# Performance work log

Measured on AMD Instinct MI355X. Metric: run time of the kernel, lower is better.

## Reference

```python
import jax, jax.numpy as jnp
import numpy as np


def setup_inputs() -> dict:
    key = jax.random.key(0)
    k1, k2 = jax.random.split(key)
    x = jax.random.normal(k1, (4, 11, 64, 96, 96), dtype=jnp.float32)
    gamma = jax.random.normal(k2, (1,), dtype=jnp.float32) * 0.1
    return {"x": x, "gamma": gamma}


def reference(x, gamma):
    # x: (B, N, C, H, W)
    B, N, C, H, W = x.shape
    q = x.reshape(B, N, C * H * W)  # (B, N, D)

    # Gram matrix: energy2[b,i,j] = <q_i, q_j>
    energy2 = jnp.einsum('bnd,bmd->bnm', q, q)  # (B, N, N)

    # Pairwise L1 distance energy1[b,i,j] = sum_d |q_i - q_j|.
    # Loop over small fixed N=11 rows to avoid a (B,N,N,D) intermediate.
    rows = [jnp.sum(jnp.abs(q - q[:, i:i + 1, :]), axis=-1) for i in range(N)]
    energy1 = jnp.stack(rows, axis=1)  # (B, N, N)
    # Original torch writes into energy1.data -> no gradient flows through it.
    energy1 = jax.lax.stop_gradient(energy1)

    energy = energy1 * energy2
    energy_new = jnp.max(energy, axis=-1, keepdims=True) - energy
    attention = jax.nn.softmax(energy_new, axis=-1)  # (B, N, N)

    out = jnp.einsum('bnm,bmd->bnd', attention, q)  # (B, N, D)
    out = out.reshape(B, N, C, H, W)
    out = gamma * out + x
    return out.reshape(B, N * C, H, W)
```

## Files before the change

### kernel.cpp

```cpp
#include <hip/hip_runtime.h>

#define B_    4
#define N_    11
#define D_    589824L
#define NPAIR 66
#define TPB   256
#define ITER  8

__global__ __launch_bounds__(TPB) void reduce_kernel(const float* __restrict__ x,
                                                     double* __restrict__ e2ws,
                                                     double* __restrict__ e1ws) {
    const int b = blockIdx.y;
    const int t = threadIdx.x;
    const long base = (long)blockIdx.x * (TPB * 4 * ITER) + (long)t * 4;
    const float* xb = x + (long)b * N_ * D_;

    float acc2[NPAIR];
    float acc1[NPAIR];
#pragma unroll
    for (int p = 0; p < NPAIR; ++p) { acc2[p] = 0.f; acc1[p] = 0.f; }

#pragma unroll 1
    for (int k = 0; k < ITER; ++k) {
        const long d = base + (long)k * (TPB * 4);
        float4 v[N_];
#pragma unroll
        for (int m = 0; m < N_; ++m)
            v[m] = *reinterpret_cast<const float4*>(xb + (long)m * D_ + d);

        int p = 0;
#pragma unroll
        for (int i = 0; i < N_; ++i) {
#pragma unroll
            for (int j = i; j < N_; ++j) {
                acc2[p] += v[i].x * v[j].x + v[i].y * v[j].y +
                           v[i].z * v[j].z + v[i].w * v[j].w;
                if (i != j) {
                    acc1[p] += fabsf(v[i].x - v[j].x) + fabsf(v[i].y - v[j].y) +
                               fabsf(v[i].z - v[j].z) + fabsf(v[i].w - v[j].w);
                }
                ++p;
            }
        }
    }

    __shared__ float red2[TPB / 64][NPAIR];
    __shared__ float red1[TPB / 64][NPAIR];
    const int wave = t >> 6, lane = t & 63;
#pragma unroll
    for (int p = 0; p < NPAIR; ++p) {
        float s2 = acc2[p], s1 = acc1[p];
#pragma unroll
        for (int off = 32; off > 0; off >>= 1) {
            s2 += __shfl_down(s2, off, 64);
            s1 += __shfl_down(s1, off, 64);
        }
        if (lane == 0) { red2[wave][p] = s2; red1[wave][p] = s1; }
    }
    __syncthreads();
    if (t < NPAIR) {
        float s2 = 0.f, s1 = 0.f;
#pragma unroll
        for (int w = 0; w < TPB / 64; ++w) { s2 += red2[w][t]; s1 += red1[w][t]; }
        atomicAdd(&e2ws[b * NPAIR + t], (double)s2);
        atomicAdd(&e1ws[b * NPAIR + t], (double)s1);
    }
}

__global__ __launch_bounds__(128) void attn_kernel(const double* __restrict__ e2ws,
                                                   const double* __restrict__ e1ws,
                                                   const float* __restrict__ gamma,
                                                   float* __restrict__ Mws) {
    const int b = blockIdx.x;
    const int t = threadIdx.x;
    __shared__ double E[N_][N_];
    if (t < NPAIR) {
        int rem = t, i = 0, cnt = N_;
        while (rem >= cnt) { rem -= cnt; --cnt; ++i; }
        const int j = i + rem;
        const double e = e1ws[b * NPAIR + t] * e2ws[b * NPAIR + t];
        E[i][j] = e;
        E[j][i] = e;
    }
    __syncthreads();
    if (t < N_) {
        const int i = t;
        double mn = E[i][0];
#pragma unroll
        for (int j = 1; j < N_; ++j) mn = fmin(mn, E[i][j]);
        double ex[N_], s = 0.0;
#pragma unroll
        for (int j = 0; j < N_; ++j) { ex[j] = exp(mn - E[i][j]); s += ex[j]; }
        const float g = gamma[0];
        const double inv = 1.0 / s;
#pragma unroll
        for (int j = 0; j < N_; ++j) {
            float m = (float)(ex[j] * inv) * g + (i == j ? 1.0f : 0.0f);
            Mws[(b * N_ + i) * N_ + j] = m;
        }
    }
}

__global__ __launch_bounds__(TPB) void apply_kernel(const float* __restrict__ x,
                                                    const float* __restrict__ Mws,
                                                    float* __restrict__ out) {
    const int b = blockIdx.y;
    const int t = threadIdx.x;
    __shared__ float M[N_ * N_];
    if (t < N_ * N_) M[t] = Mws[b * N_ * N_ + t];
    __syncthreads();

    const long d = (long)blockIdx.x * (TPB * 4) + (long)t * 4;
    const float* xb = x + (long)b * N_ * D_;
    float* ob = out + (long)b * N_ * D_;

    float4 v[N_];
#pragma unroll
    for (int m = 0; m < N_; ++m)
        v[m] = *reinterpret_cast<const float4*>(xb + (long)m * D_ + d);

#pragma unroll
    for (int n = 0; n < N_; ++n) {
        float4 o = make_float4(0.f, 0.f, 0.f, 0.f);
#pragma unroll
        for (int m = 0; m < N_; ++m) {
            const float w = M[n * N_ + m];
            o.x += w * v[m].x;
            o.y += w * v[m].y;
            o.z += w * v[m].z;
            o.w += w * v[m].w;
        }
        *reinterpret_cast<float4*>(ob + (long)n * D_ + d) = o;
    }
}

extern "C" void kernel_launch(void* const* d_in, const int* in_sizes, int n_in,
                              void* d_out, int out_size, void* d_ws, size_t ws_size,
                              hipStream_t stream) {
    const float* x     = (const float*)d_in[0];
    const float* gamma = (const float*)d_in[1];
    float* out         = (float*)d_out;

    double* e2ws = (double*)d_ws;
    double* e1ws = e2ws + B_ * NPAIR;
    float*  Mws  = (float*)(e1ws + B_ * NPAIR);

    hipMemsetAsync(d_ws, 0, (size_t)(2 * B_ * NPAIR) * sizeof(double), stream);

    dim3 gridA(D_ / (TPB * 4 * ITER), B_);
    reduce_kernel<<<gridA, TPB, 0, stream>>>(x, e2ws, e1ws);

    attn_kernel<<<B_, 128, 0, stream>>>(e2ws, e1ws, gamma, Mws);

    dim3 gridC(D_ / (TPB * 4), B_);
    apply_kernel<<<gridC, TPB, 0, stream>>>(x, Mws, out);
}
```

Measured before the change: 266.7 us.

## Trim L1 accumulators, use DPP wave reductions, raise occupancy, nontemporal output stores

The reduce kernel drops the 11 always-zero diagonal L1 accumulators, which cuts register pressure, and requests 3 waves per SIMD via launch bounds. ITER falls from 8 to 3, so more blocks are launched. The shuffle-based wave reductions become DPP row and broadcast operations, and the two LDS staging arrays merge into one. The apply kernel writes its output with nontemporal stores to reduce cache pollution. In exchange, the smaller ITER increases the number of global double atomics, and the attn kernel has to remap indices between the two accumulator layouts.

```diff
diff --git a/kernel.cpp b/kernel.cpp
--- a/kernel.cpp
+++ b/kernel.cpp
@@ -3,22 +3,37 @@
 #define B_    4
 #define N_    11
 #define D_    589824L
-#define NPAIR 66
+#define NP2   66
+#define NP1   55
+#define NRED  121
 #define TPB   256
-#define ITER  8
+#define ITER  3
 
-__global__ __launch_bounds__(TPB) void reduce_kernel(const float* __restrict__ x,
-                                                     double* __restrict__ e2ws,
-                                                     double* __restrict__ e1ws) {
+__device__ __forceinline__ float wave_red_add(float x) {
+    int t;
+    t = __builtin_amdgcn_update_dpp(0, __float_as_int(x), 0x111, 0xf, 0xf, false); x += __int_as_float(t);
+    t = __builtin_amdgcn_update_dpp(0, __float_as_int(x), 0x112, 0xf, 0xf, false); x += __int_as_float(t);
+    t = __builtin_amdgcn_update_dpp(0, __float_as_int(x), 0x114, 0xf, 0xf, false); x += __int_as_float(t);
+    t = __builtin_amdgcn_update_dpp(0, __float_as_int(x), 0x118, 0xf, 0xf, false); x += __int_as_float(t);
+    t = __builtin_amdgcn_update_dpp(0, __float_as_int(x), 0x142, 0xa, 0xf, false); x += __int_as_float(t);
+    t = __builtin_amdgcn_update_dpp(0, __float_as_int(x), 0x143, 0xc, 0xf, false); x += __int_as_float(t);
+    return x;
+}
+
+__global__ __launch_bounds__(TPB, 3) void reduce_kernel(const float* __restrict__ x,
+                                                        double* __restrict__ e2ws,
+                                                        double* __restrict__ e1ws) {
     const int b = blockIdx.y;
     const int t = threadIdx.x;
     const long base = (long)blockIdx.x * (TPB * 4 * ITER) + (long)t * 4;
     const float* xb = x + (long)b * N_ * D_;
 
-    float acc2[NPAIR];
-    float acc1[NPAIR];
+    float acc2[NP2];
+    float acc1[NP1];
 #pragma unroll
-    for (int p = 0; p < NPAIR; ++p) { acc2[p] = 0.f; acc1[p] = 0.f; }
+    for (int p = 0; p < NP2; ++p) acc2[p] = 0.f;
+#pragma unroll
+    for (int p = 0; p < NP1; ++p) acc1[p] = 0.f;
 
 #pragma unroll 1
     for (int k = 0; k < ITER; ++k) {
@@ -28,42 +43,42 @@
         for (int m = 0; m < N_; ++m)
             v[m] = *reinterpret_cast<const float4*>(xb + (long)m * D_ + d);
 
-        int p = 0;
+        int p2 = 0, p1 = 0;
 #pragma unroll
         for (int i = 0; i < N_; ++i) {
 #pragma unroll
             for (int j = i; j < N_; ++j) {
-                acc2[p] += v[i].x * v[j].x + v[i].y * v[j].y +
-                           v[i].z * v[j].z + v[i].w * v[j].w;
-                if (i != j) {
-                    acc1[p] += fabsf(v[i].x - v[j].x) + fabsf(v[i].y - v[j].y) +
-                               fabsf(v[i].z - v[j].z) + fabsf(v[i].w - v[j].w);
+                acc2[p2] += v[i].x * v[j].x + v[i].y * v[j].y +
+                            v[i].z * v[j].z + v[i].w * v[j].w;
+                ++p2;
+                if (j > i) {
+                    acc1[p1] += fabsf(v[i].x - v[j].x) + fabsf(v[i].y - v[j].y) +
+                                fabsf(v[i].z - v[j].z) + fabsf(v[i].w - v[j].w);
+                    ++p1;
                 }
-                ++p;
             }
         }
     }
 
-    __shared__ float red2[TPB / 64][NPAIR];
-    __shared__ float red1[TPB / 64][NPAIR];
+    __shared__ float red[TPB / 64][NRED];
     const int wave = t >> 6, lane = t & 63;
 #pragma unroll
-    for (int p = 0; p < NPAIR; ++p) {
-        float s2 = acc2[p], s1 = acc1[p];
+    for (int p = 0; p < NP2; ++p) {
+        const float s = wave_red_add(acc2[p]);
+        if (lane == 63) red[wave][p] = s;
+    }
 #pragma unroll
-        for (int off = 32; off > 0; off >>= 1) {
-            s2 += __shfl_down(s2, off, 64);
-            s1 += __shfl_down(s1, off, 64);
-        }
-        if (lane == 0) { red2[wave][p] = s2; red1[wave][p] = s1; }
+    for (int p = 0; p < NP1; ++p) {
+        const float s = wave_red_add(acc1[p]);
+        if (lane == 63) red[wave][NP2 + p] = s;
     }
     __syncthreads();
-    if (t < NPAIR) {
-        float s2 = 0.f, s1 = 0.f;
+    if (t < NRED) {
+        float s = 0.f;
 #pragma unroll
-        for (int w = 0; w < TPB / 64; ++w) { s2 += red2[w][t]; s1 += red1[w][t]; }
-        atomicAdd(&e2ws[b * NPAIR + t], (double)s2);
-        atomicAdd(&e1ws[b * NPAIR + t], (double)s1);
+        for (int w = 0; w < TPB / 64; ++w) s += red[w][t];
+        if (t < NP2) atomicAdd(&e2ws[b * NP2 + t], (double)s);
+        else         atomicAdd(&e1ws[b * NP1 + (t - NP2)], (double)s);
     }
 }
 
@@ -74,11 +89,15 @@
     const int b = blockIdx.x;
     const int t = threadIdx.x;
     __shared__ double E[N_][N_];
-    if (t < NPAIR) {
+    if (t < NP2) {
         int rem = t, i = 0, cnt = N_;
         while (rem >= cnt) { rem -= cnt; --cnt; ++i; }
         const int j = i + rem;
-        const double e = e1ws[b * NPAIR + t] * e2ws[b * NPAIR + t];
+        double e = 0.0;
+        if (j > i) {
+            const int q = i * (2 * N_ - 1 - i) / 2 + (j - i - 1);
+            e = e1ws[b * NP1 + q] * e2ws[b * NP2 + t];
+        }
         E[i][j] = e;
         E[j][i] = e;
     }
@@ -100,6 +119,8 @@
         }
     }
 }
+
+typedef float nfloat4 __attribute__((ext_vector_type(4)));
 
 __global__ __launch_bounds__(TPB) void apply_kernel(const float* __restrict__ x,
                                                     const float* __restrict__ Mws,
@@ -130,7 +151,9 @@
             o.z += w * v[m].z;
             o.w += w * v[m].w;
         }
-        *reinterpret_cast<float4*>(ob + (long)n * D_ + d) = o;
+        union { float4 f; nfloat4 n4; } u;
+        u.f = o;
+        __builtin_nontemporal_store(u.n4, reinterpret_cast<nfloat4*>(ob + (long)n * D_ + d));
     }
 }
 
@@ -142,10 +165,10 @@
     float* out         = (float*)d_out;
 
     double* e2ws = (double*)d_ws;
-    double* e1ws = e2ws + B_ * NPAIR;
-    float*  Mws  = (float*)(e1ws + B_ * NPAIR);
+    double* e1ws = e2ws + B_ * NP2;
+    float*  Mws  = (float*)(e1ws + B_ * NP1);
 
-    hipMemsetAsync(d_ws, 0, (size_t)(2 * B_ * NPAIR) * sizeof(double), stream);
+    hipMemsetAsync(d_ws, 0, (size_t)(B_ * (NP2 + NP1)) * sizeof(double), stream);
 
     dim3 gridA(D_ / (TPB * 4 * ITER), B_);
     reduce_kernel<<<gridA, TPB, 0, stream>>>(x, e2ws, e1ws);
```

Measured after the change: 318.4 us. +19.4%, slower.
